# Kernel optimization log

Hardware: AMD Instinct MI355X
Metric: run time of the kernel (lower is better)

Reference implementation:

```python
import jax, jax.numpy as jnp
import numpy as np

_HMT = np.array([[1, 1, 1, 1], [1, -1, 1, -1], [1, 1, -1, -1], [1, -1, -1, 1]], dtype=np.float32)
_H = jnp.asarray(_HMT)
_H2 = jnp.asarray(_HMT[[1, 0, 2, 3], :])
_H3 = jnp.asarray(_HMT[[3, 1, 2, 0], :])
# inverse-transform rows 1:3 (2x4), reconstructed from truncated source
_IH = _H[1:3, :]
_IH2 = _H2[1:3, :]
_IH3 = _H3[1:3, :]

KERNEL = 4
STRIDE = 2


def setup_inputs() -> dict:
    key = jax.random.key(0)
    k1, k2, k3 = jax.random.split(key, 3)
    B, Cin, Cout, ih, iw = 16, 64, 96, 128, 128
    x = jax.random.normal(k1, (B, Cin, ih, iw), dtype=jnp.float32)
    weight = jax.random.normal(k2, (Cout, Cin, KERNEL, KERNEL), dtype=jnp.float32) * 0.05
    bias = jax.random.normal(k3, (1, Cout, 1, 1), dtype=jnp.float32) * 0.05
    return {"x": x, "weight": weight, "bias": bias}


def _extract_patches(xp, nH, nW):
    # patches[b,c,i,j,u,v] = xp[b,c, 2i+v, 2j+u]  (torch unfold(3).unfold(2) order)
    idx_h = 2 * np.arange(nH)[:, None] + np.arange(KERNEL)[None, :]  # (nH,4) over (i,v)
    idx_w = 2 * np.arange(nW)[:, None] + np.arange(KERNEL)[None, :]  # (nW,4) over (j,u)
    return xp[:, :, idx_h[:, None, None, :], idx_w[None, :, :, None]]  # (B,C,nH,nW,4,4)


def _group(t, w, ih_mat):
    # t: (B,C,nH,nW,4,4) transform-domain patches; w: (Og,C,4,4)
    m = jnp.einsum('bcijuv,ocuv->boijuv', t, w)
    # IH @ m @ IH.T -> (B,Og,nH,nW,2,2)
    return jnp.einsum('pu,boijuv,qv->boijpq', ih_mat, m, ih_mat)


def reference(x, weight, bias):
    B, Cin, ih, iw = x.shape
    Cout = weight.shape[0]
    nH, nW = ih // STRIDE, iw // STRIDE
    xp = jnp.pad(x, ((0, 0), (0, 0), (1, 1), (1, 1)))
    patches = _extract_patches(xp, nH, nW)
    # forward transforms: H @ P @ H ; H2.T @ P @ H2 ; H3.T @ P @ H3
    t1 = jnp.einsum('au,bcijuv,vd->bcijad', _H, patches, _H)
    t2 = jnp.einsum('ua,bcijuv,vd->bcijad', _H2, patches, _H2)
    t3 = jnp.einsum('ua,bcijuv,vd->bcijad', _H3, patches, _H3)
    g = Cout // 3
    h1 = _group(t1, weight[:g], _IH)
    h2 = _group(t2, weight[g:2 * g], _IH2)
    h3 = _group(t3, weight[2 * g:], _IH3)
    hmult = jnp.concatenate([h1, h2, h3], axis=1)  # (B,Cout,nH,nW,2,2)
    # out[b,o,2i+p,2j+q] = hmult[b,o,i,j,p,q]
    out = hmult.transpose(0, 1, 2, 4, 3, 5).reshape(B, Cout, ih, iw)
    return out + bias
```

## Files before the change

### kernel.cpp

```cpp
#include <hip/hip_runtime.h>
#include <hip/hip_bf16.h>
#include <cstddef>
#include <cstdint>


#define IHW 128
#define CIN 64
#define COUT 96
#define NCK 16
#define P_DW 168
#define COFF_DW 80
#define XBUF_DW (12 * P_DW)
#define ABUF_DW 4096

typedef __attribute__((ext_vector_type(8))) short short8_t;
typedef __attribute__((ext_vector_type(4))) float floatx4;

__device__ __forceinline__ short bf16r(float f) {
  uint32_t u = __float_as_uint(f);
  uint32_t r = (u + 0x7FFFu + ((u >> 16) & 1u)) >> 16;
  return (short)r;
}

__device__ __forceinline__ uint32_t pk(float lo, float hi) {
  union { __hip_bfloat16 h; unsigned short s; } a, bq;
  a.h = __float2bfloat16(lo);
  bq.h = __float2bfloat16(hi);
  return (uint32_t)a.s | ((uint32_t)bq.s << 16);
}

__global__ void keff_kernel(const float* __restrict__ w, short* __restrict__ keff) {
  int idx = blockIdx.x * 256 + threadIdx.x;
  if (idx >= COUT * CIN) return;
  int o = idx / CIN, c = idx % CIN;
  int g = o / 32;

  int perm[4] = {0, 1, 2, 3};
  if (g == 1) { perm[0] = 1; perm[1] = 0; }
  else if (g == 2) { perm[0] = 3; perm[3] = 0; }

  const float H[4][4] = {{1,1,1,1},{1,-1,1,-1},{1,1,-1,-1},{1,-1,-1,1}};
  float S[2][4];
#pragma unroll
  for (int p = 0; p < 2; ++p)
#pragma unroll
    for (int a = 0; a < 4; ++a) {
      bool pos = (g == 1) ? ((p == 0) ? true : (a < 2))
                          : ((p == 0) ? ((a & 1) == 0) : (a < 2));
      S[p][a] = pos ? 1.f : -1.f;
    }

  float wv[4][4];
#pragma unroll
  for (int a = 0; a < 4; ++a)
#pragma unroll
    for (int d = 0; d < 4; ++d) wv[a][d] = w[(o * CIN + c) * 16 + a * 4 + d];

  for (int p = 0; p < 2; ++p)
    for (int q = 0; q < 2; ++q) {
      int n = o * 4 + p * 2 + q;
      for (int y = 0; y < 4; ++y)
        for (int xx = 0; xx < 4; ++xx) {
          float s = 0.f;
#pragma unroll
          for (int a = 0; a < 4; ++a) {
            float ea = S[p][a] * H[a][perm[xx]];
#pragma unroll
            for (int d = 0; d < 4; ++d) s += ea * S[q][d] * H[d][perm[y]] * wv[a][d];
          }
          keff[n * 1024 + c * 16 + y * 4 + xx] = bf16r(s);
        }
    }
}

__global__ __launch_bounds__(256) void conv_mfma(const float* __restrict__ x,
                                                 const short* __restrict__ keff,
                                                 const float* __restrict__ bias,
                                                 float* __restrict__ out) {
  __shared__ uint32_t xlds[2 * XBUF_DW];
  __shared__ uint32_t alds[2 * ABUF_DW];

  const int tid = threadIdx.x;
  const int lane = tid & 63;
  const int wid = tid >> 6;
  const int wavem = wid >> 1;
  const int wn = wid & 1;
  const int l15 = lane & 15;
  const int l4 = lane >> 4;

  const int hw = blockIdx.x;
  const int xcd = hw & 7;
  const int r = hw >> 3;
  const int tile = xcd * 64 + r / 3;
  const int nblk = r % 3;
  const int b = tile >> 5;
  const int ib = tile & 31;
  const int gy0 = ib * 4 - 1;

  const float* xb = x + (size_t)b * CIN * IHW * IHW;

  int sl_off[3], sl_dw[3], sl_s[3];
  bool sl_ok[3];
#pragma unroll
  for (int it = 0; it < 3; ++it) {
    const int slot = tid + it * 256;
    const int seg = slot >> 5;
    const int s = slot & 31;
    const int c_sub = seg / 12;
    const int rr = seg % 12;
    const int kk2 = rr / 6;
    const int y = rr % 6;
    const int c_loc = 2 * kk2 + c_sub;
    const int gy = gy0 + y;
    const bool ok = (unsigned)gy < (unsigned)IHW;
    sl_off[it] = (c_loc * IHW + (ok ? gy : 0)) * IHW + 4 * s;
    sl_dw[it] = rr * P_DW + c_sub * COFF_DW;
    sl_s[it] = s;
    sl_ok[it] = ok;
  }

  int aoff[4];
#pragma unroll
  for (int it = 0; it < 4; ++it) {
    const int slot = tid + it * 256;
    const int n = slot >> 3;
    const int u = slot & 7;
    aoff[it] = (nblk * 128 + n) * 1024 + ((u ^ (n & 7)) << 3);
  }

  float4 gv[3];
  float gn[3];
#define ISSUE(ckv)                                                        \
  {                                                                       \
    _Pragma("unroll") for (int it = 0; it < 3; ++it) {                    \
      const float* p = xb + sl_off[it] + (size_t)(ckv) * (4 * IHW * IHW); \
      gv[it] = *reinterpret_cast<const float4*>(p);                       \
      gn[it] = (sl_s[it] < 31) ? p[4] : 0.f;                              \
    }                                                                     \
  }

#define WRITEST(bs)                                                       \
  {                                                                       \
    uint32_t* Bp = xlds + (bs) * XBUF_DW;                                 \
    _Pragma("unroll") for (int it = 0; it < 3; ++it) {                    \
      float4 v = gv[it];                                                  \
      float nx = gn[it];                                                  \
      if (!sl_ok[it]) { v.x = 0.f; v.y = 0.f; v.z = 0.f; v.w = 0.f; nx = 0.f; } \
      const int o = sl_dw[it] + 2 * sl_s[it] + 1;                         \
      Bp[o] = pk(v.y, v.z);                                               \
      Bp[o + 1] = pk(v.w, nx);                                            \
      if (sl_s[it] == 0) Bp[sl_dw[it]] = pk(0.f, v.x);                    \
    }                                                                     \
  }

#define ADMA(bs, ckv)                                                     \
  {                                                                       \
    _Pragma("unroll") for (int it = 0; it < 4; ++it) {                    \
      const short* src = keff + aoff[it] + (ckv) * 64;                    \
      __builtin_amdgcn_global_load_lds(                                   \
          (const __attribute__((address_space(1))) void*)src,             \
          (__attribute__((address_space(3))) void*)                       \
              &alds[(bs) * ABUF_DW + (tid + it * 256) * 4],               \
          16, 0, 0);                                                      \
    }                                                                     \
  }

  union ufrag { short8_t s8; uint32_t u[4]; };

#define KKSTEP(Apt, Xkt, abase)                                           \
  {                                                                       \
    short8_t af[4];                                                       \
    _Pragma("unroll") for (int nf = 0; nf < 4; ++nf)                      \
      af[nf] = *reinterpret_cast<const short8_t*>((Apt) + (abase) + nf * 512); \
    ufrag xf[4];                                                          \
    _Pragma("unroll") for (int mf = 0; mf < 4; ++mf) {                    \
      xf[mf].u[0] = (Xkt)[mf * 16];                                       \
      xf[mf].u[1] = (Xkt)[mf * 16 + 1];                                   \
      xf[mf].u[2] = (Xkt)[mf * 16 + P_DW];                                \
      xf[mf].u[3] = (Xkt)[mf * 16 + P_DW + 1];                            \
    }                                                                     \
    __builtin_amdgcn_s_setprio(1);                                        \
    _Pragma("unroll") for (int mf = 0; mf < 4; ++mf)                      \
      _Pragma("unroll") for (int nf = 0; nf < 4; ++nf)                    \
        acc[mf][nf] = __builtin_amdgcn_mfma_f32_16x16x32_bf16(            \
            af[nf], xf[mf].s8, acc[mf][nf], 0, 0, 0);                     \
    __builtin_amdgcn_s_setprio(0);                                        \
  }

  floatx4 acc[4][4];
#pragma unroll
  for (int i = 0; i < 4; ++i)
#pragma unroll
    for (int j2 = 0; j2 < 4; ++j2) acc[i][j2] = (floatx4){0.f, 0.f, 0.f, 0.f};

  float biasr[4];
#pragma unroll
  for (int nf = 0; nf < 4; ++nf) biasr[nf] = bias[nblk * 32 + wn * 16 + nf * 4 + l4];

  const int cm_dw = (2 * wavem + 2 * (l4 & 1)) * P_DW + (l4 >> 1) * COFF_DW + l15;
  const int a0 = (wn * 64 + l15) * 32 + ((l4 ^ (l15 & 7)) << 2);
  const int a1 = a0 ^ 16;

  ISSUE(0);
  ADMA(0, 0);
  WRITEST(0);
  ISSUE(1);

  for (int ck = 0; ck < NCK - 1; ++ck) {
    asm volatile("s_waitcnt vmcnt(6) lgkmcnt(0)" ::: "memory");
    __builtin_amdgcn_s_barrier();
    __builtin_amdgcn_sched_barrier(0);

    const int cur = ck & 1;
    const uint32_t* Ap = alds + cur * ABUF_DW;
    const uint32_t* Xk0 = xlds + cur * XBUF_DW + cm_dw;
    const uint32_t* Xk1 = Xk0 + 6 * P_DW;

    ADMA(cur ^ 1, ck + 1);
    KKSTEP(Ap, Xk0, a0);
    KKSTEP(Ap, Xk1, a1);
    WRITEST(cur ^ 1);
    if (ck + 2 < NCK) ISSUE(ck + 2);
  }

  asm volatile("s_waitcnt vmcnt(0) lgkmcnt(0)" ::: "memory");
  __builtin_amdgcn_s_barrier();
  __builtin_amdgcn_sched_barrier(0);
  {
    const uint32_t* Ap = alds + ABUF_DW;
    const uint32_t* Xk0 = xlds + XBUF_DW + cm_dw;
    const uint32_t* Xk1 = Xk0 + 6 * P_DW;
    KKSTEP(Ap, Xk0, a0);
    KKSTEP(Ap, Xk1, a1);
  }

  const int i_row = ib * 2 + wavem;
  const int orow0 = 2 * i_row;
#pragma unroll
  for (int nf = 0; nf < 4; ++nf) {
    const int o = nblk * 32 + wn * 16 + nf * 4 + l4;
    const float bv = biasr[nf];
    float* obase = out + ((size_t)(b * COUT + o) * IHW + orow0) * IHW;
#pragma unroll
    for (int mf = 0; mf < 4; ++mf) {
      const int col = 2 * (mf * 16 + l15);
      float2 s0 = make_float2(acc[mf][nf][0] + bv, acc[mf][nf][1] + bv);
      float2 s1 = make_float2(acc[mf][nf][2] + bv, acc[mf][nf][3] + bv);
      *reinterpret_cast<float2*>(obase + col) = s0;
      *reinterpret_cast<float2*>(obase + IHW + col) = s1;
    }
  }
#undef ISSUE
#undef WRITEST
#undef ADMA
#undef KKSTEP
}

extern "C" void kernel_launch(void* const* d_in, const int* in_sizes, int n_in,
                              void* d_out, int out_size, void* d_ws, size_t ws_size,
                              hipStream_t stream) {
  const float* x = (const float*)d_in[0];
  const float* w = (const float*)d_in[1];
  const float* bias = (const float*)d_in[2];
  float* out = (float*)d_out;
  short* keff = (short*)d_ws;

  hipLaunchKernelGGL(keff_kernel, dim3(24), dim3(256), 0, stream, w, keff);
  hipLaunchKernelGGL(conv_mfma, dim3(1536), dim3(256), 0, stream, x, keff, bias, out);
}
```

Before: 81.75 us.

## Add bf16 padded-image prepass and direct-to-LDS input loads

Adds a prepass kernel that converts the fp32 input into a zero-padded bf16 image in workspace. The conv kernel can then stage input tiles straight into LDS with global_load_lds instead of loading through registers, converting and scattering them. This removes per-block conversion and register traffic in the main loop and halves the input bytes read there. In exchange it adds an extra kernel launch plus a full write and re-read of the image, uses a simpler synchronous wait (vmcnt(0)) pipeline, and keeps the old kernel as a fallback when the workspace is too small.

```diff
diff --git a/kernel.cpp b/kernel.cpp
--- a/kernel.cpp
+++ b/kernel.cpp
@@ -8,10 +8,6 @@
 #define CIN 64
 #define COUT 96
 #define NCK 16
-#define P_DW 168
-#define COFF_DW 80
-#define XBUF_DW (12 * P_DW)
-#define ABUF_DW 4096
 
 typedef __attribute__((ext_vector_type(8))) short short8_t;
 typedef __attribute__((ext_vector_type(4))) float floatx4;
@@ -73,11 +69,185 @@
     }
 }
 
-__global__ __launch_bounds__(256) void conv_mfma(const float* __restrict__ x,
+__global__ __launch_bounds__(256) void prepass(const float* __restrict__ x,
+                                               uint32_t* __restrict__ img) {
+  const int u = blockIdx.x * 256 + threadIdx.x;
+  const int u17 = u % 17;
+  const int r = u / 17;
+  const int py = r % 130;
+  const int rc = r / 130;
+  uint32_t d0 = 0, d1 = 0, d2 = 0, d3 = 0;
+  if (py != 0 && py != 129) {
+    const float* xrow = x + ((size_t)rc * IHW + (py - 1)) * IHW;
+    const int pc0 = u17 * 8;
+    float v[8];
+#pragma unroll
+    for (int e = 0; e < 8; ++e) {
+      const int gx = pc0 + e - 1;
+      v[e] = ((unsigned)gx < (unsigned)IHW) ? xrow[gx] : 0.f;
+    }
+    d0 = pk(v[0], v[1]); d1 = pk(v[2], v[3]);
+    d2 = pk(v[4], v[5]); d3 = pk(v[6], v[7]);
+  }
+  uint4* dst = reinterpret_cast<uint4*>(img + (size_t)r * 68 + u17 * 4);
+  *dst = make_uint4(d0, d1, d2, d3);
+}
+
+#define XBUF_DW 1632
+#define ABUF_DW 4096
+
+__global__ __launch_bounds__(256) void conv_mfma(const uint32_t* __restrict__ img,
                                                  const short* __restrict__ keff,
                                                  const float* __restrict__ bias,
                                                  float* __restrict__ out) {
   __shared__ uint32_t xlds[2 * XBUF_DW];
+  __shared__ uint32_t alds[2 * ABUF_DW];
+
+  const int tid = threadIdx.x;
+  const int lane = tid & 63;
+  const int wid = tid >> 6;
+  const int wavem = wid >> 1;
+  const int wn = wid & 1;
+  const int l15 = lane & 15;
+  const int l4 = lane >> 4;
+
+  const int hw = blockIdx.x;
+  const int xcd = hw & 7;
+  const int r = hw >> 3;
+  const int tile = xcd * 64 + r / 3;
+  const int nblk = r % 3;
+  const int b = tile >> 5;
+  const int ib = tile & 31;
+
+  const uint32_t* imgb = img + (size_t)b * CIN * 130 * 68;
+
+  int xsrc[2];
+  bool xok[2];
+#pragma unroll
+  for (int it = 0; it < 2; ++it) {
+    const int u = wid * 102 + lane + it * 64;
+    const int ri = u / 17;
+    const int col16 = u % 17;
+    const int kk = ri / 12;
+    const int rem = ri % 12;
+    const int y = rem >> 1;
+    const int cs = rem & 1;
+    const int cl = 2 * kk + cs;
+    xsrc[it] = (cl * 130 + 4 * ib + y) * 68 + col16 * 4;
+    xok[it] = (it == 0) || (lane < 38);
+  }
+
+  int aoff[4];
+#pragma unroll
+  for (int it = 0; it < 4; ++it) {
+    const int slot = tid + it * 256;
+    const int n = slot >> 3;
+    const int u = slot & 7;
+    aoff[it] = (nblk * 128 + n) * 1024 + ((u ^ (n & 7)) << 3);
+  }
+
+#define STAGE(bs, ckv)                                                     \
+  {                                                                        \
+    _Pragma("unroll") for (int it = 0; it < 4; ++it) {                     \
+      const short* src = keff + aoff[it] + (ckv) * 64;                     \
+      __builtin_amdgcn_global_load_lds(                                    \
+          (const __attribute__((address_space(1))) void*)src,              \
+          (__attribute__((address_space(3))) void*)                        \
+              &alds[(bs) * ABUF_DW + (tid + it * 256) * 4],                \
+          16, 0, 0);                                                       \
+    }                                                                      \
+    _Pragma("unroll") for (int it = 0; it < 2; ++it) {                     \
+      if (xok[it]) {                                                       \
+        const uint32_t* src = imgb + xsrc[it] + (ckv) * (4 * 130 * 68);    \
+        __builtin_amdgcn_global_load_lds(                                  \
+            (const __attribute__((address_space(1))) void*)src,            \
+            (__attribute__((address_space(3))) void*)                      \
+                &xlds[(bs) * XBUF_DW + (wid * 102 + it * 64) * 4],         \
+            16, 0, 0);                                                     \
+      }                                                                    \
+    }                                                                      \
+  }
+
+  union ufrag { short8_t s8; uint32_t u[4]; };
+
+  floatx4 acc[4][4];
+#pragma unroll
+  for (int i2 = 0; i2 < 4; ++i2)
+#pragma unroll
+    for (int j2 = 0; j2 < 4; ++j2) acc[i2][j2] = (floatx4){0.f, 0.f, 0.f, 0.f};
+
+  float biasr[4];
+#pragma unroll
+  for (int nf = 0; nf < 4; ++nf) biasr[nf] = bias[nblk * 32 + wn * 16 + nf * 4 + l4];
+
+  const int xbase = (4 * wavem + 4 * (l4 & 1) + (l4 >> 1)) * 68 + l15;
+  const int abase = (wn * 64 + l15) * 32 + ((l4 ^ (l15 & 7)) << 2);
+
+#define COMPUTE(ckv)                                                       \
+  {                                                                        \
+    const uint32_t* Ap = alds + ((ckv) & 1) * ABUF_DW;                     \
+    const uint32_t* Xp = xlds + ((ckv) & 1) * XBUF_DW + xbase;             \
+    _Pragma("unroll") for (int kk = 0; kk < 2; ++kk) {                     \
+      short8_t af[4];                                                      \
+      _Pragma("unroll") for (int nf = 0; nf < 4; ++nf)                     \
+        af[nf] = *reinterpret_cast<const short8_t*>(                       \
+            Ap + (abase ^ (kk << 4)) + nf * 512);                          \
+      const uint32_t* Xk = Xp + kk * 816;                                  \
+      ufrag xf[4];                                                         \
+      _Pragma("unroll") for (int mf = 0; mf < 4; ++mf) {                   \
+        const int o = mf * 16;                                             \
+        xf[mf].u[0] = Xk[o];                                               \
+        xf[mf].u[1] = Xk[o + 1];                                           \
+        xf[mf].u[2] = Xk[o + 136];                                         \
+        xf[mf].u[3] = Xk[o + 137];                                         \
+      }                                                                    \
+      _Pragma("unroll") for (int mf = 0; mf < 4; ++mf)                     \
+        _Pragma("unroll") for (int nf = 0; nf < 4; ++nf)                   \
+          acc[mf][nf] = __builtin_amdgcn_mfma_f32_16x16x32_bf16(           \
+              af[nf], xf[mf].s8, acc[mf][nf], 0, 0, 0);                    \
+    }                                                                      \
+  }
+
+  STAGE(0, 0);
+
+  for (int ck = 0; ck < NCK; ++ck) {
+    asm volatile("s_waitcnt vmcnt(0) lgkmcnt(0)" ::: "memory");
+    __builtin_amdgcn_s_barrier();
+    __builtin_amdgcn_sched_barrier(0);
+    if (ck < NCK - 1) STAGE((ck + 1) & 1, ck + 1);
+    __builtin_amdgcn_sched_barrier(0);
+    COMPUTE(ck);
+  }
+
+  const int i_row = ib * 2 + wavem;
+  const int orow0 = 2 * i_row;
+#pragma unroll
+  for (int nf = 0; nf < 4; ++nf) {
+    const int o = nblk * 32 + wn * 16 + nf * 4 + l4;
+    const float bv = biasr[nf];
+    float* obase = out + ((size_t)(b * COUT + o) * IHW + orow0) * IHW;
+#pragma unroll
+    for (int mf = 0; mf < 4; ++mf) {
+      const int col = 2 * (mf * 16 + l15);
+      float2 s0 = make_float2(acc[mf][nf][0] + bv, acc[mf][nf][1] + bv);
+      float2 s1 = make_float2(acc[mf][nf][2] + bv, acc[mf][nf][3] + bv);
+      *reinterpret_cast<float2*>(obase + col) = s0;
+      *reinterpret_cast<float2*>(obase + IHW + col) = s1;
+    }
+  }
+#undef STAGE
+#undef COMPUTE
+}
+
+#define FB_P_DW 168
+#define FB_COFF 80
+#define FB_XBUF (12 * FB_P_DW)
+
+__global__ __launch_bounds__(256) void conv_fb(const float* __restrict__ x,
+                                               const short* __restrict__ keff,
+                                               const float* __restrict__ bias,
+                                               float* __restrict__ out) {
+  __shared__ uint32_t xlds[2 * FB_XBUF];
   __shared__ uint32_t alds[2 * ABUF_DW];
 
   const int tid = threadIdx.x;
@@ -114,7 +284,7 @@
     const int gy = gy0 + y;
     const bool ok = (unsigned)gy < (unsigned)IHW;
     sl_off[it] = (c_loc * IHW + (ok ? gy : 0)) * IHW + 4 * s;
-    sl_dw[it] = rr * P_DW + c_sub * COFF_DW;
+    sl_dw[it] = rr * FB_P_DW + c_sub * FB_COFF;
     sl_s[it] = s;
     sl_ok[it] = ok;
   }
@@ -130,7 +300,7 @@
 
   float4 gv[3];
   float gn[3];
-#define ISSUE(ckv)                                                        \
+#define FISSUE(ckv)                                                       \
   {                                                                       \
     _Pragma("unroll") for (int it = 0; it < 3; ++it) {                    \
       const float* p = xb + sl_off[it] + (size_t)(ckv) * (4 * IHW * IHW); \
@@ -138,10 +308,9 @@
       gn[it] = (sl_s[it] < 31) ? p[4] : 0.f;                              \
     }                                                                     \
   }
-
-#define WRITEST(bs)                                                       \
+#define FWRITE(bs)                                                        \
   {                                                                       \
-    uint32_t* Bp = xlds + (bs) * XBUF_DW;                                 \
+    uint32_t* Bp = xlds + (bs) * FB_XBUF;                                 \
     _Pragma("unroll") for (int it = 0; it < 3; ++it) {                    \
       float4 v = gv[it];                                                  \
       float nx = gn[it];                                                  \
@@ -152,8 +321,7 @@
       if (sl_s[it] == 0) Bp[sl_dw[it]] = pk(0.f, v.x);                    \
     }                                                                     \
   }
-
-#define ADMA(bs, ckv)                                                     \
+#define FADMA(bs, ckv)                                                    \
   {                                                                       \
     _Pragma("unroll") for (int it = 0; it < 4; ++it) {                    \
       const short* src = keff + aoff[it] + (ckv) * 64;                    \
@@ -165,73 +333,67 @@
     }                                                                     \
   }
 
-  union ufrag { short8_t s8; uint32_t u[4]; };
-
-#define KKSTEP(Apt, Xkt, abase)                                           \
+  union ufragf { short8_t s8; uint32_t u[4]; };
+#define FKK(Apt, Xkt, abasev)                                             \
   {                                                                       \
     short8_t af[4];                                                       \
     _Pragma("unroll") for (int nf = 0; nf < 4; ++nf)                      \
-      af[nf] = *reinterpret_cast<const short8_t*>((Apt) + (abase) + nf * 512); \
-    ufrag xf[4];                                                          \
+      af[nf] = *reinterpret_cast<const short8_t*>((Apt) + (abasev) + nf * 512); \
+    ufragf xf[4];                                                         \
     _Pragma("unroll") for (int mf = 0; mf < 4; ++mf) {                    \
       xf[mf].u[0] = (Xkt)[mf * 16];                                       \
       xf[mf].u[1] = (Xkt)[mf * 16 + 1];                                   \
-      xf[mf].u[2] = (Xkt)[mf * 16 + P_DW];                                \
-      xf[mf].u[3] = (Xkt)[mf * 16 + P_DW + 1];                            \
+      xf[mf].u[2] = (Xkt)[mf * 16 + FB_P_DW];                             \
+      xf[mf].u[3] = (Xkt)[mf * 16 + FB_P_DW + 1];                         \
     }                                                                     \
-    __builtin_amdgcn_s_setprio(1);                                        \
     _Pragma("unroll") for (int mf = 0; mf < 4; ++mf)                      \
       _Pragma("unroll") for (int nf = 0; nf < 4; ++nf)                    \
         acc[mf][nf] = __builtin_amdgcn_mfma_f32_16x16x32_bf16(            \
             af[nf], xf[mf].s8, acc[mf][nf], 0, 0, 0);                     \
-    __builtin_amdgcn_s_setprio(0);                                        \
   }
 
   floatx4 acc[4][4];
 #pragma unroll
-  for (int i = 0; i < 4; ++i)
-#pragma unroll
-    for (int j2 = 0; j2 < 4; ++j2) acc[i][j2] = (floatx4){0.f, 0.f, 0.f, 0.f};
+  for (int i2 = 0; i2 < 4; ++i2)
+#pragma unroll
+    for (int j2 = 0; j2 < 4; ++j2) acc[i2][j2] = (floatx4){0.f, 0.f, 0.f, 0.f};
 
   float biasr[4];
 #pragma unroll
   for (int nf = 0; nf < 4; ++nf) biasr[nf] = bias[nblk * 32 + wn * 16 + nf * 4 + l4];
 
-  const int cm_dw = (2 * wavem + 2 * (l4 & 1)) * P_DW + (l4 >> 1) * COFF_DW + l15;
+  const int cm_dw = (2 * wavem + 2 * (l4 & 1)) * FB_P_DW + (l4 >> 1) * FB_COFF + l15;
   const int a0 = (wn * 64 + l15) * 32 + ((l4 ^ (l15 & 7)) << 2);
   const int a1 = a0 ^ 16;
 
-  ISSUE(0);
-  ADMA(0, 0);
-  WRITEST(0);
-  ISSUE(1);
+  FISSUE(0);
+  FADMA(0, 0);
+  FWRITE(0);
+  FISSUE(1);
 
   for (int ck = 0; ck < NCK - 1; ++ck) {
     asm volatile("s_waitcnt vmcnt(6) lgkmcnt(0)" ::: "memory");
     __builtin_amdgcn_s_barrier();
     __builtin_amdgcn_sched_barrier(0);
-
     const int cur = ck & 1;
     const uint32_t* Ap = alds + cur * ABUF_DW;
-    const uint32_t* Xk0 = xlds + cur * XBUF_DW + cm_dw;
-    const uint32_t* Xk1 = Xk0 + 6 * P_DW;
-
-    ADMA(cur ^ 1, ck + 1);
-    KKSTEP(Ap, Xk0, a0);
-    KKSTEP(Ap, Xk1, a1);
-    WRITEST(cur ^ 1);
-    if (ck + 2 < NCK) ISSUE(ck + 2);
-  }
-
+    const uint32_t* Xk0 = xlds + cur * FB_XBUF + cm_dw;
+    const uint32_t* Xk1 = Xk0 + 6 * FB_P_DW;
+    FADMA(cur ^ 1, ck + 1);
+    FKK(Ap, Xk0, a0);
+    FKK(Ap, Xk1, a1);
+    FWRITE(cur ^ 1);
+    if (ck + 2 < NCK) FISSUE(ck + 2);
+  }
   asm volatile("s_waitcnt vmcnt(0) lgkmcnt(0)" ::: "memory");
   __builtin_amdgcn_s_barrier();
   __builtin_amdgcn_sched_barrier(0);
   {
     const uint32_t* Ap = alds + ABUF_DW;
-    const uint32_t* Xk0 = xlds + XBUF_DW + cm_dw;
-    const uint32_t* Xk1 = Xk0 + 6 * P_DW;
-    KKSTEP(Ap, Xk0, a0);
-    KKSTEP(Ap, Xk1, a1);
+    const uint32_t* Xk0 = xlds + FB_XBUF + cm_dw;
+    const uint32_t* Xk1 = Xk0 + 6 * FB_P_DW;
+    FKK(Ap, Xk0, a0);
+    FKK(Ap, Xk1, a1);
   }
 
   const int i_row = ib * 2 + wavem;
@@ -250,10 +412,10 @@
       *reinterpret_cast<float2*>(obase + IHW + col) = s1;
     }
   }
-#undef ISSUE
-#undef WRITEST
-#undef ADMA
-#undef KKSTEP
+#undef FISSUE
+#undef FWRITE
+#undef FADMA
+#undef FKK
 }
 
 extern "C" void kernel_launch(void* const* d_in, const int* in_sizes, int n_in,
@@ -264,7 +426,15 @@
   const float* bias = (const float*)d_in[2];
   float* out = (float*)d_out;
   short* keff = (short*)d_ws;
+  uint32_t* img = (uint32_t*)((char*)d_ws + 786432);
+
+  const size_t NEED = 786432 + (size_t)16 * 64 * 130 * 272;
 
   hipLaunchKernelGGL(keff_kernel, dim3(24), dim3(256), 0, stream, w, keff);
-  hipLaunchKernelGGL(conv_mfma, dim3(1536), dim3(256), 0, stream, x, keff, bias, out);
-}
+  if (ws_size >= NEED) {
+    hipLaunchKernelGGL(prepass, dim3(8840), dim3(256), 0, stream, x, img);
+    hipLaunchKernelGGL(conv_mfma, dim3(1536), dim3(256), 0, stream, img, keff, bias, out);
+  } else {
+    hipLaunchKernelGGL(conv_fb, dim3(1536), dim3(256), 0, stream, x, keff, bias, out);
+  }
+}
```

New measurement: 105.0 us. 28.4% more time.
